# Performance work log

Hardware: AMD Instinct MI355X
Metric: run time of the kernel (lower is better)

Reference implementation:

```python
import jax, jax.numpy as jnp
import numpy as np

B, S, D = 2, 2048, 1024
H = 16
HD = D // H  # head_dim = 64


def setup_inputs() -> dict:
    key = jax.random.key(0)
    ks = jax.random.split(key, 9)
    sc_in = 1.0 / np.sqrt(D)
    return {
        "x": jax.random.normal(ks[0], (B, S, D), dtype=jnp.float32),
        "Wq": jax.random.normal(ks[1], (D, D), dtype=jnp.float32) * sc_in,
        "bq": jnp.zeros((D,), dtype=jnp.float32),
        "Wk": jax.random.normal(ks[2], (D, D), dtype=jnp.float32) * sc_in,
        "bk": jnp.zeros((D,), dtype=jnp.float32),
        "Wv": jax.random.normal(ks[3], (D, D), dtype=jnp.float32) * sc_in,
        "bv": jnp.zeros((D,), dtype=jnp.float32),
        "Wo": jax.random.normal(ks[4], (D, D), dtype=jnp.float32) * sc_in,
        "bo": jnp.zeros((D,), dtype=jnp.float32),
    }


def reference(x, Wq, bq, Wk, bk, Wv, bv, Wo, bo):
    # QKV projections: [B,S,D] -> [B,H,S,HD]
    def split_heads(t):
        return t.reshape(B, S, H, HD).transpose(0, 2, 1, 3)

    Q = split_heads(x @ Wq + bq)
    K = split_heads(x @ Wk + bk)
    V = split_heads(x @ Wv + bv)

    scale = 1.0 / np.sqrt(HD).astype(np.float32)
    scores = jnp.einsum("bhqd,bhkd->bhqk", Q, K) * scale  # [B,H,S,S]
    weights = jax.nn.softmax(scores, axis=-1)
    # dropout(p=0.1) is identity in eval mode
    attended = jnp.einsum("bhqk,bhkd->bhqd", weights, V)  # [B,H,S,HD]
    attended = attended.transpose(0, 2, 1, 3).reshape(B, S, D)
    return attended @ Wo + bo
```

## Files before the change

kernel.cpp:

```cpp
#include <hip/hip_runtime.h>
#include <hip/hip_bf16.h>


#define S_ 2048
#define D_ 1024
#define HD_ 64
#define LDSW 72
#define QSZ 4194304
#define LOG2E 1.44269504f

typedef __attribute__((ext_vector_type(8))) short bf16x8;
typedef __attribute__((ext_vector_type(4))) float f32x4;

static __device__ __forceinline__ short f2bs(float f) {
    __hip_bfloat16 h = __float2bfloat16(f);
    return *reinterpret_cast<short*>(&h);
}
static __device__ __forceinline__ float bs2f(short s) {
    __hip_bfloat16 h = *reinterpret_cast<__hip_bfloat16*>(&s);
    return __bfloat162float(h);
}
static __device__ __forceinline__ bf16x8 cvt8(const float* p) {
    f32x4 u0 = *(const f32x4*)p;
    f32x4 u1 = *(const f32x4*)(p + 4);
    bf16x8 r;
    r[0] = f2bs(u0[0]); r[1] = f2bs(u0[1]); r[2] = f2bs(u0[2]); r[3] = f2bs(u0[3]);
    r[4] = f2bs(u1[0]); r[5] = f2bs(u1[1]); r[6] = f2bs(u1[2]); r[7] = f2bs(u1[3]);
    return r;
}
static __device__ __forceinline__ void gld16(const void* g, void* l) {
    __builtin_amdgcn_global_load_lds(
        (const __attribute__((address_space(1))) unsigned int*)g,
        (__attribute__((address_space(3))) unsigned int*)l, 16, 0, 0);
}
static __device__ __forceinline__ int detect_f32(const unsigned int* __restrict__ xw) {
    const unsigned int w = xw[threadIdx.x & 63];
    const int e = (int)((w >> 7) & 0xFFu);
    unsigned long long m = __ballot(e >= 117 && e <= 130);
    return (__popcll(m) >= 32) ? 0 : 1;
}

__global__ __launch_bounds__(256) void prep(
    const void* __restrict__ x,
    const void* __restrict__ w0, const void* __restrict__ w1,
    const void* __restrict__ w2, const void* __restrict__ w3,
    short* __restrict__ Wt)
{
    __shared__ __align__(16) short Ts[64 * LDSW];
    const int f32in = detect_f32((const unsigned int*)x);
    const int idx = blockIdx.x;
    const int z = idx >> 8, bb = idx & 255;
    const void* W = z == 0 ? w0 : z == 1 ? w1 : z == 2 ? w2 : w3;
    short* O = Wt + (size_t)z * D_ * D_;
    const int k0 = (bb & 15) * 64, n0 = (bb >> 4) * 64;
    const int t = threadIdx.x;
    const int row = t >> 2, seg = t & 3;

    if (f32in) {
        const float* wg = (const float*)W + (size_t)(k0 + row) * D_ + n0;
        *(bf16x8*)&Ts[row * LDSW + seg * 8]      = cvt8(wg + seg * 8);
        *(bf16x8*)&Ts[row * LDSW + seg * 8 + 32] = cvt8(wg + seg * 8 + 32);
    } else {
        const short* wg = (const short*)W + (size_t)(k0 + row) * D_ + n0;
        *(bf16x8*)&Ts[row * LDSW + seg * 8]      = *(const bf16x8*)(wg + seg * 8);
        *(bf16x8*)&Ts[row * LDSW + seg * 8 + 32] = *(const bf16x8*)(wg + seg * 8 + 32);
    }
    __syncthreads();

    short* og = O + (size_t)(n0 + row) * D_ + k0;
    #pragma unroll
    for (int g = 0; g < 2; ++g) {
        const int ks = seg * 8 + g * 32;
        alignas(16) short tmp[8];
        #pragma unroll
        for (int i = 0; i < 8; ++i) tmp[i] = Ts[(ks + i) * LDSW + row];
        *(bf16x8*)(og + ks) = *(const bf16x8*)tmp;
    }
}

__global__ __launch_bounds__(256) void gemm_qkv(
    const void* __restrict__ X, const short* __restrict__ Wt3,
    const void* __restrict__ bq, const void* __restrict__ bk,
    const void* __restrict__ bv, short* __restrict__ out)
{
    __shared__ __align__(16) short As[128 * 64];
    __shared__ __align__(16) short Bs[128 * 64];
    const int ext_f32 = detect_f32((const unsigned int*)X);
    const int t = threadIdx.x;
    const int wave = t >> 6, lane = t & 63;
    const int quad = lane >> 4, l16 = lane & 15;
    const int wm = wave & 1, wn = wave >> 1;
    const int m0 = blockIdx.x * 128, n0 = blockIdx.y * 128;
    const int id = n0 >> 10;
    const int lr = lane >> 3;
    const int kx = ((lane & 7) ^ (lr & 7)) * 8;

    f32x4 acc[4][4];
    #pragma unroll
    for (int i = 0; i < 4; ++i)
        #pragma unroll
        for (int j = 0; j < 4; ++j) acc[i][j] = (f32x4){0.f, 0.f, 0.f, 0.f};

    const size_t arow = (size_t)(m0 + wave * 32 + lr) * D_ + kx;
    const short* Bb = Wt3 + (size_t)(n0 + wave * 32 + lr) * D_ + kx;

    for (int kb = 0; kb < 16; ++kb) {
        __syncthreads();
        const int k0 = kb * 64;
        if (ext_f32) {
            const float* Xf = (const float*)X;
            #pragma unroll
            for (int i = 0; i < 4; ++i)
                *(bf16x8*)&As[(wave * 4 + i) * 512 + lane * 8] =
                    cvt8(Xf + arow + (size_t)i * 8 * D_ + k0);
        } else {
            const short* Xs = (const short*)X;
            #pragma unroll
            for (int i = 0; i < 4; ++i)
                gld16(Xs + arow + (size_t)i * 8 * D_ + k0, &As[(wave * 4 + i) * 512]);
        }
        #pragma unroll
        for (int i = 0; i < 4; ++i)
            gld16(Bb + (size_t)i * 8 * D_ + k0, &Bs[(wave * 4 + i) * 512]);
        __syncthreads();

        #pragma unroll
        for (int ks = 0; ks < 2; ++ks) {
            const int sw = ((ks * 4 + quad) ^ (l16 & 7)) * 8;
            bf16x8 af[4], bfr[4];
            #pragma unroll
            for (int i = 0; i < 4; ++i) {
                af[i]  = *(const bf16x8*)&As[(wm * 64 + i * 16 + l16) * 64 + sw];
                bfr[i] = *(const bf16x8*)&Bs[(wn * 64 + i * 16 + l16) * 64 + sw];
            }
            #pragma unroll
            for (int mi = 0; mi < 4; ++mi)
                #pragma unroll
                for (int ni = 0; ni < 4; ++ni)
                    acc[mi][ni] = __builtin_amdgcn_mfma_f32_16x16x32_bf16(
                        af[mi], bfr[ni], acc[mi][ni], 0, 0, 0);
        }
    }

    const void* bias = id == 0 ? bq : id == 1 ? bk : bv;
    const float oscale = id == 0 ? 0.125f : 1.0f;
    #pragma unroll
    for (int ni = 0; ni < 4; ++ni) {
        const int n = n0 + wn * 64 + ni * 16 + l16;
        const int nl = n & 1023, h = nl >> 6, d = nl & 63;
        const float bvl = ext_f32 ? ((const float*)bias)[nl]
                                  : bs2f(((const short*)bias)[nl]);
        #pragma unroll
        for (int mi = 0; mi < 4; ++mi)
            #pragma unroll
            for (int r = 0; r < 4; ++r) {
                const int m = m0 + wm * 64 + mi * 16 + quad * 4 + r;
                const int b = m >> 11, s = m & 2047;
                const int bh = b * 16 + h;
                const float v = (acc[mi][ni][r] + bvl) * oscale;
                const size_t idx = (id < 2)
                    ? (size_t)id * QSZ + ((size_t)bh * S_ + s) * HD_ + d
                    : (size_t)2 * QSZ + ((size_t)bh * HD_ + d) * S_ + s;
                out[idx] = f2bs(v);
            }
    }
}

__global__ __launch_bounds__(256) void gemm_out(
    const short* __restrict__ A, const short* __restrict__ Bt,
    const void* __restrict__ bias, void* __restrict__ C,
    const unsigned int* __restrict__ xw)
{
    __shared__ __align__(16) short As[64 * 64];
    __shared__ __align__(16) short Bs[128 * 64];
    const int ext_f32 = detect_f32(xw);
    const int t = threadIdx.x;
    const int wave = t >> 6, lane = t & 63;
    const int quad = lane >> 4, l16 = lane & 15;
    const int wm = wave & 1, wn = wave >> 1;
    const int m0 = blockIdx.x * 64, n0 = blockIdx.y * 128;
    const int lr = lane >> 3;
    const int kx = ((lane & 7) ^ (lr & 7)) * 8;

    f32x4 acc[2][4];
    #pragma unroll
    for (int i = 0; i < 2; ++i)
        #pragma unroll
        for (int j = 0; j < 4; ++j) acc[i][j] = (f32x4){0.f, 0.f, 0.f, 0.f};

    const short* Ab = A  + (size_t)(m0 + wave * 16 + lr) * D_ + kx;
    const short* Bb = Bt + (size_t)(n0 + wave * 32 + lr) * D_ + kx;

    for (int kb = 0; kb < 16; ++kb) {
        __syncthreads();
        const int k0 = kb * 64;
        #pragma unroll
        for (int i = 0; i < 2; ++i)
            gld16(Ab + (size_t)i * 8 * D_ + k0, &As[(wave * 2 + i) * 512]);
        #pragma unroll
        for (int i = 0; i < 4; ++i)
            gld16(Bb + (size_t)i * 8 * D_ + k0, &Bs[(wave * 4 + i) * 512]);
        __syncthreads();

        #pragma unroll
        for (int ks = 0; ks < 2; ++ks) {
            const int sw = ((ks * 4 + quad) ^ (l16 & 7)) * 8;
            bf16x8 af[2], bfr[4];
            #pragma unroll
            for (int i = 0; i < 2; ++i)
                af[i] = *(const bf16x8*)&As[(wm * 32 + i * 16 + l16) * 64 + sw];
            #pragma unroll
            for (int i = 0; i < 4; ++i)
                bfr[i] = *(const bf16x8*)&Bs[(wn * 64 + i * 16 + l16) * 64 + sw];
            #pragma unroll
            for (int mi = 0; mi < 2; ++mi)
                #pragma unroll
                for (int ni = 0; ni < 4; ++ni)
                    acc[mi][ni] = __builtin_amdgcn_mfma_f32_16x16x32_bf16(
                        af[mi], bfr[ni], acc[mi][ni], 0, 0, 0);
        }
    }

    #pragma unroll
    for (int ni = 0; ni < 4; ++ni) {
        const int n = n0 + wn * 64 + ni * 16 + l16;
        const float bvl = ext_f32 ? ((const float*)bias)[n]
                                  : bs2f(((const short*)bias)[n]);
        #pragma unroll
        for (int mi = 0; mi < 2; ++mi)
            #pragma unroll
            for (int r = 0; r < 4; ++r) {
                const int m = m0 + wm * 32 + mi * 16 + quad * 4 + r;
                const float v = acc[mi][ni][r] + bvl;
                const size_t idx = (size_t)m * D_ + n;
                if (ext_f32) ((float*)C)[idx] = v;
                else         ((short*)C)[idx] = f2bs(v);
            }
    }
}

__global__ __launch_bounds__(256) void attn(
    const short* __restrict__ Q, const short* __restrict__ K,
    const short* __restrict__ Vt, short* __restrict__ Aout)
{
    __shared__ __align__(16) short Ks[64 * 64];
    __shared__ __align__(16) short Vs[64 * 64];
    __shared__ __align__(16) short Ps[4][32 * LDSW];

    const int t = threadIdx.x;
    const int wave = t >> 6, lane = t & 63;
    const int quad = lane >> 4, l16 = lane & 15;
    const int bh = blockIdx.x;
    const int q0 = blockIdx.y * 128;
    const int lr = lane >> 3;
    const int kx = ((lane & 7) ^ (lr & 7)) * 8;
    short* pw = &Ps[wave][0];

    bf16x8 bq[2][2];
    #pragma unroll
    for (int mi = 0; mi < 2; ++mi) {
        const short* qr = Q + ((size_t)bh * S_ + q0 + wave * 32 + mi * 16 + l16) * HD_ + quad * 8;
        bq[mi][0] = *(const bf16x8*)qr;
        bq[mi][1] = *(const bf16x8*)(qr + 32);
    }

    bf16x8 ones;
    #pragma unroll
    for (int i = 0; i < 8; ++i) ones[i] = (short)0x3F80;

    f32x4 o[2][4], lacc[2];
    #pragma unroll
    for (int mi = 0; mi < 2; ++mi) {
        lacc[mi] = (f32x4){0.f, 0.f, 0.f, 0.f};
        #pragma unroll
        for (int nt = 0; nt < 4; ++nt) o[mi][nt] = (f32x4){0.f, 0.f, 0.f, 0.f};
    }

    const short* Kb = K  + ((size_t)bh * S_  + wave * 16 + lr) * HD_ + kx;
    const short* Vb = Vt + ((size_t)bh * HD_ + wave * 16 + lr) * S_ + kx;

    for (int j = 0; j < 32; ++j) {
        __syncthreads();
        #pragma unroll
        for (int i = 0; i < 2; ++i) {
            gld16(Kb + ((size_t)j * 64 + i * 8) * HD_, &Ks[(wave * 2 + i) * 512]);
            gld16(Vb + (size_t)i * 8 * S_ + j * 64,    &Vs[(wave * 2 + i) * 512]);
        }
        __syncthreads();

        f32x4 st[2][4];
        #pragma unroll
        for (int nt = 0; nt < 4; ++nt) {
            bf16x8 kf0 = *(const bf16x8*)&Ks[(nt * 16 + l16) * 64 + ((quad ^ (l16 & 7)) * 8)];
            bf16x8 kf1 = *(const bf16x8*)&Ks[(nt * 16 + l16) * 64 + (((4 + quad) ^ (l16 & 7)) * 8)];
            #pragma unroll
            for (int mi = 0; mi < 2; ++mi) {
                f32x4 z = (f32x4){0.f, 0.f, 0.f, 0.f};
                z = __builtin_amdgcn_mfma_f32_16x16x32_bf16(kf0, bq[mi][0], z, 0, 0, 0);
                z = __builtin_amdgcn_mfma_f32_16x16x32_bf16(kf1, bq[mi][1], z, 0, 0, 0);
                st[mi][nt] = z;
            }
        }

        #pragma unroll
        for (int mi = 0; mi < 2; ++mi)
            #pragma unroll
            for (int nt = 0; nt < 4; ++nt) {
                unsigned u0 = __float_as_uint(__builtin_amdgcn_exp2f(st[mi][nt][0] * LOG2E));
                unsigned u1 = __float_as_uint(__builtin_amdgcn_exp2f(st[mi][nt][1] * LOG2E));
                unsigned u2 = __float_as_uint(__builtin_amdgcn_exp2f(st[mi][nt][2] * LOG2E));
                unsigned u3 = __float_as_uint(__builtin_amdgcn_exp2f(st[mi][nt][3] * LOG2E));
                uint2 pk;
                pk.x = __builtin_amdgcn_perm(u1, u0, 0x07060302);
                pk.y = __builtin_amdgcn_perm(u3, u2, 0x07060302);
                *(uint2*)&pw[(mi * 16 + l16) * LDSW + nt * 16 + quad * 4] = pk;
            }
        __builtin_amdgcn_s_waitcnt(0xc07f);

        #pragma unroll
        for (int ks = 0; ks < 2; ++ks) {
            bf16x8 vf[4];
            #pragma unroll
            for (int nt = 0; nt < 4; ++nt)
                vf[nt] = *(const bf16x8*)&Vs[(nt * 16 + l16) * 64 + (((ks * 4 + quad) ^ (l16 & 7)) * 8)];
            #pragma unroll
            for (int mi = 0; mi < 2; ++mi) {
                bf16x8 ap = *(const bf16x8*)&pw[(mi * 16 + l16) * LDSW + ks * 32 + quad * 8];
                lacc[mi] = __builtin_amdgcn_mfma_f32_16x16x32_bf16(ap, ones, lacc[mi], 0, 0, 0);
                #pragma unroll
                for (int nt = 0; nt < 4; ++nt)
                    o[mi][nt] = __builtin_amdgcn_mfma_f32_16x16x32_bf16(ap, vf[nt], o[mi][nt], 0, 0, 0);
            }
        }
    }

    const int b = bh >> 4, h = bh & 15;
    #pragma unroll
    for (int mi = 0; mi < 2; ++mi)
        #pragma unroll
        for (int r = 0; r < 4; ++r) {
            const float inv = 1.f / lacc[mi][r];
            const int s = q0 + wave * 32 + mi * 16 + quad * 4 + r;
            const size_t base = ((size_t)b * S_ + s) * D_ + h * HD_;
            #pragma unroll
            for (int nt = 0; nt < 4; ++nt)
                Aout[base + nt * 16 + l16] = f2bs(o[mi][nt][r] * inv);
        }
}

extern "C" void kernel_launch(void* const* d_in, const int* in_sizes, int n_in,
                              void* d_out, int out_size, void* d_ws, size_t ws_size,
                              hipStream_t stream) {
    char* ws = (char*)d_ws;
    short* Wt  = (short*)(ws + ((size_t)1  << 20));
    short* Att = (short*)(ws + ((size_t)9  << 20));
    short* QKV = (short*)(ws + ((size_t)17 << 20));
    const unsigned int* xw = (const unsigned int*)d_in[0];

    prep<<<1024, 256, 0, stream>>>(d_in[0], d_in[1], d_in[3], d_in[5], d_in[7], Wt);
    gemm_qkv<<<dim3(32, 24), 256, 0, stream>>>(d_in[0], Wt, d_in[2], d_in[4], d_in[6], QKV);
    attn<<<dim3(32, 16), 256, 0, stream>>>(QKV, QKV + QSZ, QKV + 2 * QSZ, Att);
    gemm_out<<<dim3(64, 8), 256, 0, stream>>>(Att, Wt + (3 << 20), d_in[8], d_out, xw);
}
```

Baseline: 190.5 us.

## Double-buffer K/V tiles in attention, use 8 waves, fold log2e into Q scale

The attention kernel now runs 512 threads per block, with each wave owning 16 query rows instead of 32. K and V tiles are double-buffered in shared memory so the next tile's global load is issued before compute on the current one, which leaves one barrier per iteration. The log2(e) factor is folded into the Q projection scale, removing a multiply per exponent. The cost is twice the LDS for K/V, fewer MFMAs per wave relative to its K/V fragment loads, and more waves competing for registers and LDS.

New measurement: 188.8 us (median of 2 runs). About the same (-0.9%).

```diff
diff --git a/kernel.cpp b/kernel.cpp
--- a/kernel.cpp
+++ b/kernel.cpp
@@ -7,7 +7,6 @@
 #define HD_ 64
 #define LDSW 72
 #define QSZ 4194304
-#define LOG2E 1.44269504f
 
 typedef __attribute__((ext_vector_type(8))) short bf16x8;
 typedef __attribute__((ext_vector_type(4))) float f32x4;
@@ -143,7 +142,7 @@
     }
 
     const void* bias = id == 0 ? bq : id == 1 ? bk : bv;
-    const float oscale = id == 0 ? 0.125f : 1.0f;
+    const float oscale = id == 0 ? 0.18033688011112042f : 1.0f;
     #pragma unroll
     for (int ni = 0; ni < 4; ++ni) {
         const int n = n0 + wn * 64 + ni * 16 + l16;
@@ -239,13 +238,13 @@
     }
 }
 
-__global__ __launch_bounds__(256) void attn(
+__global__ __launch_bounds__(512) void attn(
     const short* __restrict__ Q, const short* __restrict__ K,
     const short* __restrict__ Vt, short* __restrict__ Aout)
 {
-    __shared__ __align__(16) short Ks[64 * 64];
-    __shared__ __align__(16) short Vs[64 * 64];
-    __shared__ __align__(16) short Ps[4][32 * LDSW];
+    __shared__ __align__(16) short Ks[2][64 * 64];
+    __shared__ __align__(16) short Vs[2][64 * 64];
+    __shared__ __align__(16) short Ps[8][16 * LDSW];
 
     const int t = threadIdx.x;
     const int wave = t >> 6, lane = t & 63;
@@ -256,65 +255,58 @@
     const int kx = ((lane & 7) ^ (lr & 7)) * 8;
     short* pw = &Ps[wave][0];
 
-    bf16x8 bq[2][2];
-    #pragma unroll
-    for (int mi = 0; mi < 2; ++mi) {
-        const short* qr = Q + ((size_t)bh * S_ + q0 + wave * 32 + mi * 16 + l16) * HD_ + quad * 8;
-        bq[mi][0] = *(const bf16x8*)qr;
-        bq[mi][1] = *(const bf16x8*)(qr + 32);
+    bf16x8 bq0, bq1;
+    {
+        const short* qr = Q + ((size_t)bh * S_ + q0 + wave * 16 + l16) * HD_ + quad * 8;
+        bq0 = *(const bf16x8*)qr;
+        bq1 = *(const bf16x8*)(qr + 32);
     }
 
     bf16x8 ones;
     #pragma unroll
     for (int i = 0; i < 8; ++i) ones[i] = (short)0x3F80;
 
-    f32x4 o[2][4], lacc[2];
-    #pragma unroll
-    for (int mi = 0; mi < 2; ++mi) {
-        lacc[mi] = (f32x4){0.f, 0.f, 0.f, 0.f};
-        #pragma unroll
-        for (int nt = 0; nt < 4; ++nt) o[mi][nt] = (f32x4){0.f, 0.f, 0.f, 0.f};
-    }
-
-    const short* Kb = K  + ((size_t)bh * S_  + wave * 16 + lr) * HD_ + kx;
-    const short* Vb = Vt + ((size_t)bh * HD_ + wave * 16 + lr) * S_ + kx;
+    f32x4 o[4], lacc;
+    lacc = (f32x4){0.f, 0.f, 0.f, 0.f};
+    #pragma unroll
+    for (int nt = 0; nt < 4; ++nt) o[nt] = (f32x4){0.f, 0.f, 0.f, 0.f};
+
+    const short* Kb = K  + ((size_t)bh * S_  + wave * 8 + lr) * HD_ + kx;
+    const short* Vb = Vt + ((size_t)bh * HD_ + wave * 8 + lr) * S_ + kx;
+
+    gld16(Kb, &Ks[0][wave * 512]);
+    gld16(Vb, &Vs[0][wave * 512]);
+    __syncthreads();
 
     for (int j = 0; j < 32; ++j) {
-        __syncthreads();
-        #pragma unroll
-        for (int i = 0; i < 2; ++i) {
-            gld16(Kb + ((size_t)j * 64 + i * 8) * HD_, &Ks[(wave * 2 + i) * 512]);
-            gld16(Vb + (size_t)i * 8 * S_ + j * 64,    &Vs[(wave * 2 + i) * 512]);
-        }
-        __syncthreads();
-
-        f32x4 st[2][4];
+        const int cur = j & 1;
+        if (j < 31) {
+            gld16(Kb + (size_t)((j + 1) * 64) * HD_, &Ks[cur ^ 1][wave * 512]);
+            gld16(Vb + (j + 1) * 64,                 &Vs[cur ^ 1][wave * 512]);
+        }
+
+        f32x4 st[4];
         #pragma unroll
         for (int nt = 0; nt < 4; ++nt) {
-            bf16x8 kf0 = *(const bf16x8*)&Ks[(nt * 16 + l16) * 64 + ((quad ^ (l16 & 7)) * 8)];
-            bf16x8 kf1 = *(const bf16x8*)&Ks[(nt * 16 + l16) * 64 + (((4 + quad) ^ (l16 & 7)) * 8)];
-            #pragma unroll
-            for (int mi = 0; mi < 2; ++mi) {
-                f32x4 z = (f32x4){0.f, 0.f, 0.f, 0.f};
-                z = __builtin_amdgcn_mfma_f32_16x16x32_bf16(kf0, bq[mi][0], z, 0, 0, 0);
-                z = __builtin_amdgcn_mfma_f32_16x16x32_bf16(kf1, bq[mi][1], z, 0, 0, 0);
-                st[mi][nt] = z;
-            }
-        }
-
-        #pragma unroll
-        for (int mi = 0; mi < 2; ++mi)
-            #pragma unroll
-            for (int nt = 0; nt < 4; ++nt) {
-                unsigned u0 = __float_as_uint(__builtin_amdgcn_exp2f(st[mi][nt][0] * LOG2E));
-                unsigned u1 = __float_as_uint(__builtin_amdgcn_exp2f(st[mi][nt][1] * LOG2E));
-                unsigned u2 = __float_as_uint(__builtin_amdgcn_exp2f(st[mi][nt][2] * LOG2E));
-                unsigned u3 = __float_as_uint(__builtin_amdgcn_exp2f(st[mi][nt][3] * LOG2E));
-                uint2 pk;
-                pk.x = __builtin_amdgcn_perm(u1, u0, 0x07060302);
-                pk.y = __builtin_amdgcn_perm(u3, u2, 0x07060302);
-                *(uint2*)&pw[(mi * 16 + l16) * LDSW + nt * 16 + quad * 4] = pk;
-            }
+            bf16x8 kf0 = *(const bf16x8*)&Ks[cur][(nt * 16 + l16) * 64 + ((quad ^ (l16 & 7)) * 8)];
+            bf16x8 kf1 = *(const bf16x8*)&Ks[cur][(nt * 16 + l16) * 64 + (((4 + quad) ^ (l16 & 7)) * 8)];
+            f32x4 z = (f32x4){0.f, 0.f, 0.f, 0.f};
+            z = __builtin_amdgcn_mfma_f32_16x16x32_bf16(kf0, bq0, z, 0, 0, 0);
+            z = __builtin_amdgcn_mfma_f32_16x16x32_bf16(kf1, bq1, z, 0, 0, 0);
+            st[nt] = z;
+        }
+
+        #pragma unroll
+        for (int nt = 0; nt < 4; ++nt) {
+            unsigned u0 = __float_as_uint(__builtin_amdgcn_exp2f(st[nt][0]));
+            unsigned u1 = __float_as_uint(__builtin_amdgcn_exp2f(st[nt][1]));
+            unsigned u2 = __float_as_uint(__builtin_amdgcn_exp2f(st[nt][2]));
+            unsigned u3 = __float_as_uint(__builtin_amdgcn_exp2f(st[nt][3]));
+            uint2 pk;
+            pk.x = __builtin_amdgcn_perm(u1, u0, 0x07060302);
+            pk.y = __builtin_amdgcn_perm(u3, u2, 0x07060302);
+            *(uint2*)&pw[l16 * LDSW + nt * 16 + quad * 4] = pk;
+        }
         __builtin_amdgcn_s_waitcnt(0xc07f);
 
         #pragma unroll
@@ -322,30 +314,27 @@
             bf16x8 vf[4];
             #pragma unroll
             for (int nt = 0; nt < 4; ++nt)
-                vf[nt] = *(const bf16x8*)&Vs[(nt * 16 + l16) * 64 + (((ks * 4 + quad) ^ (l16 & 7)) * 8)];
-            #pragma unroll
-            for (int mi = 0; mi < 2; ++mi) {
-                bf16x8 ap = *(const bf16x8*)&pw[(mi * 16 + l16) * LDSW + ks * 32 + quad * 8];
-                lacc[mi] = __builtin_amdgcn_mfma_f32_16x16x32_bf16(ap, ones, lacc[mi], 0, 0, 0);
-                #pragma unroll
-                for (int nt = 0; nt < 4; ++nt)
-                    o[mi][nt] = __builtin_amdgcn_mfma_f32_16x16x32_bf16(ap, vf[nt], o[mi][nt], 0, 0, 0);
-            }
-        }
+                vf[nt] = *(const bf16x8*)&Vs[cur][(nt * 16 + l16) * 64 + (((ks * 4 + quad) ^ (l16 & 7)) * 8)];
+            bf16x8 ap = *(const bf16x8*)&pw[l16 * LDSW + ks * 32 + quad * 8];
+            lacc = __builtin_amdgcn_mfma_f32_16x16x32_bf16(ap, ones, lacc, 0, 0, 0);
+            #pragma unroll
+            for (int nt = 0; nt < 4; ++nt)
+                o[nt] = __builtin_amdgcn_mfma_f32_16x16x32_bf16(ap, vf[nt], o[nt], 0, 0, 0);
+        }
+
+        __syncthreads();
     }
 
     const int b = bh >> 4, h = bh & 15;
     #pragma unroll
-    for (int mi = 0; mi < 2; ++mi)
-        #pragma unroll
-        for (int r = 0; r < 4; ++r) {
-            const float inv = 1.f / lacc[mi][r];
-            const int s = q0 + wave * 32 + mi * 16 + quad * 4 + r;
-            const size_t base = ((size_t)b * S_ + s) * D_ + h * HD_;
-            #pragma unroll
-            for (int nt = 0; nt < 4; ++nt)
-                Aout[base + nt * 16 + l16] = f2bs(o[mi][nt][r] * inv);
-        }
+    for (int r = 0; r < 4; ++r) {
+        const float inv = 1.f / lacc[r];
+        const int s = q0 + wave * 16 + quad * 4 + r;
+        const size_t base = ((size_t)b * S_ + s) * D_ + h * HD_;
+        #pragma unroll
+        for (int nt = 0; nt < 4; ++nt)
+            Aout[base + nt * 16 + l16] = f2bs(o[nt][r] * inv);
+    }
 }
 
 extern "C" void kernel_launch(void* const* d_in, const int* in_sizes, int n_in,
@@ -359,6 +348,6 @@
 
     prep<<<1024, 256, 0, stream>>>(d_in[0], d_in[1], d_in[3], d_in[5], d_in[7], Wt);
     gemm_qkv<<<dim3(32, 24), 256, 0, stream>>>(d_in[0], Wt, d_in[2], d_in[4], d_in[6], QKV);
-    attn<<<dim3(32, 16), 256, 0, stream>>>(QKV, QKV + QSZ, QKV + 2 * QSZ, Att);
+    attn<<<dim3(32, 16), 512, 0, stream>>>(QKV, QKV + QSZ, QKV + 2 * QSZ, Att);
     gemm_out<<<dim3(64, 8), 256, 0, stream>>>(Att, Wt + (3 << 20), d_in[8], d_out, xw);
 }
```

## Double-buffer K/V tiles and feed P from registers via 16x16x16 MFMA

Applied to the files above, without the earlier changes.

The attention loop now double-buffers the K and V tiles in LDS, prefetching the next tile while the current one is computed, and uses one barrier per iteration instead of two. The softmax numerator P is no longer staged through LDS. The S^T=K·Q layout is used directly as the A operand of 16x16x16 bf16 MFMAs, which removes the per-wave P buffer, its store/load and the waitcnt. The log2(e) factor is folded into the Q projection scale so the exp2 no longer needs a multiply. In exchange there are twice as many (smaller) MFMA instructions for PV and the row sums, and twice the LDS for K/V.

Result: slower. 201.1 us (+5.6%).

```diff
diff --git a/kernel.cpp b/kernel.cpp
--- a/kernel.cpp
+++ b/kernel.cpp
@@ -7,9 +7,9 @@
 #define HD_ 64
 #define LDSW 72
 #define QSZ 4194304
-#define LOG2E 1.44269504f
 
 typedef __attribute__((ext_vector_type(8))) short bf16x8;
+typedef __attribute__((ext_vector_type(4))) short bf16x4;
 typedef __attribute__((ext_vector_type(4))) float f32x4;
 
 static __device__ __forceinline__ short f2bs(float f) {
@@ -27,6 +27,14 @@
     r[0] = f2bs(u0[0]); r[1] = f2bs(u0[1]); r[2] = f2bs(u0[2]); r[3] = f2bs(u0[3]);
     r[4] = f2bs(u1[0]); r[5] = f2bs(u1[1]); r[6] = f2bs(u1[2]); r[7] = f2bs(u1[3]);
     return r;
+}
+static __device__ __forceinline__ f32x4 pmfma(bf16x4 a, bf16x4 b, f32x4 c) {
+#if __has_builtin(__builtin_amdgcn_mfma_f32_16x16x16bf16_1k)
+    return __builtin_amdgcn_mfma_f32_16x16x16bf16_1k(a, b, c, 0, 0, 0);
+#else
+    asm("v_mfma_f32_16x16x16_bf16 %0, %1, %2, %0" : "+v"(c) : "v"(a), "v"(b));
+    return c;
+#endif
 }
 static __device__ __forceinline__ void gld16(const void* g, void* l) {
     __builtin_amdgcn_global_load_lds(
@@ -143,7 +151,7 @@
     }
 
     const void* bias = id == 0 ? bq : id == 1 ? bk : bv;
-    const float oscale = id == 0 ? 0.125f : 1.0f;
+    const float oscale = id == 0 ? 0.18033688011112042f : 1.0f;
     #pragma unroll
     for (int ni = 0; ni < 4; ++ni) {
         const int n = n0 + wn * 64 + ni * 16 + l16;
@@ -243,9 +251,8 @@
     const short* __restrict__ Q, const short* __restrict__ K,
     const short* __restrict__ Vt, short* __restrict__ Aout)
 {
-    __shared__ __align__(16) short Ks[64 * 64];
-    __shared__ __align__(16) short Vs[64 * 64];
-    __shared__ __align__(16) short Ps[4][32 * LDSW];
+    __shared__ __align__(16) short Ks[2][64 * 64];
+    __shared__ __align__(16) short Vs[2][64 * 64];
 
     const int t = threadIdx.x;
     const int wave = t >> 6, lane = t & 63;
@@ -254,7 +261,8 @@
     const int q0 = blockIdx.y * 128;
     const int lr = lane >> 3;
     const int kx = ((lane & 7) ^ (lr & 7)) * 8;
-    short* pw = &Ps[wave][0];
+    const int x7 = l16 & 7;
+    const int qh = quad >> 1, ql = (quad & 1) * 4;
 
     bf16x8 bq[2][2];
     #pragma unroll
@@ -264,9 +272,9 @@
         bq[mi][1] = *(const bf16x8*)(qr + 32);
     }
 
-    bf16x8 ones;
-    #pragma unroll
-    for (int i = 0; i < 8; ++i) ones[i] = (short)0x3F80;
+    bf16x4 ones4;
+    #pragma unroll
+    for (int i = 0; i < 4; ++i) ones4[i] = (short)0x3F80;
 
     f32x4 o[2][4], lacc[2];
     #pragma unroll
@@ -279,59 +287,64 @@
     const short* Kb = K  + ((size_t)bh * S_  + wave * 16 + lr) * HD_ + kx;
     const short* Vb = Vt + ((size_t)bh * HD_ + wave * 16 + lr) * S_ + kx;
 
+    #pragma unroll
+    for (int i = 0; i < 2; ++i) {
+        gld16(Kb + (size_t)i * 8 * HD_, &Ks[0][(wave * 2 + i) * 512]);
+        gld16(Vb + (size_t)i * 8 * S_,  &Vs[0][(wave * 2 + i) * 512]);
+    }
+    __syncthreads();
+
     for (int j = 0; j < 32; ++j) {
-        __syncthreads();
-        #pragma unroll
-        for (int i = 0; i < 2; ++i) {
-            gld16(Kb + ((size_t)j * 64 + i * 8) * HD_, &Ks[(wave * 2 + i) * 512]);
-            gld16(Vb + (size_t)i * 8 * S_ + j * 64,    &Vs[(wave * 2 + i) * 512]);
-        }
-        __syncthreads();
-
-        f32x4 st[2][4];
+        const int cur = j & 1;
+        if (j < 31) {
+            #pragma unroll
+            for (int i = 0; i < 2; ++i) {
+                gld16(Kb + (size_t)((j + 1) * 64 + i * 8) * HD_, &Ks[cur ^ 1][(wave * 2 + i) * 512]);
+                gld16(Vb + (size_t)i * 8 * S_ + (j + 1) * 64,    &Vs[cur ^ 1][(wave * 2 + i) * 512]);
+            }
+        }
+        const short* Kc = &Ks[cur][0];
+        const short* Vc = &Vs[cur][0];
+
+        bf16x4 pa[2][4];
         #pragma unroll
         for (int nt = 0; nt < 4; ++nt) {
-            bf16x8 kf0 = *(const bf16x8*)&Ks[(nt * 16 + l16) * 64 + ((quad ^ (l16 & 7)) * 8)];
-            bf16x8 kf1 = *(const bf16x8*)&Ks[(nt * 16 + l16) * 64 + (((4 + quad) ^ (l16 & 7)) * 8)];
+            bf16x8 kf0 = *(const bf16x8*)&Kc[(nt * 16 + l16) * 64 + ((quad ^ x7) * 8)];
+            bf16x8 kf1 = *(const bf16x8*)&Kc[(nt * 16 + l16) * 64 + (((4 + quad) ^ x7) * 8)];
             #pragma unroll
             for (int mi = 0; mi < 2; ++mi) {
                 f32x4 z = (f32x4){0.f, 0.f, 0.f, 0.f};
                 z = __builtin_amdgcn_mfma_f32_16x16x32_bf16(kf0, bq[mi][0], z, 0, 0, 0);
                 z = __builtin_amdgcn_mfma_f32_16x16x32_bf16(kf1, bq[mi][1], z, 0, 0, 0);
-                st[mi][nt] = z;
-            }
-        }
-
-        #pragma unroll
-        for (int mi = 0; mi < 2; ++mi)
-            #pragma unroll
-            for (int nt = 0; nt < 4; ++nt) {
-                unsigned u0 = __float_as_uint(__builtin_amdgcn_exp2f(st[mi][nt][0] * LOG2E));
-                unsigned u1 = __float_as_uint(__builtin_amdgcn_exp2f(st[mi][nt][1] * LOG2E));
-                unsigned u2 = __float_as_uint(__builtin_amdgcn_exp2f(st[mi][nt][2] * LOG2E));
-                unsigned u3 = __float_as_uint(__builtin_amdgcn_exp2f(st[mi][nt][3] * LOG2E));
+                unsigned u0 = __float_as_uint(__builtin_amdgcn_exp2f(z[0]));
+                unsigned u1 = __float_as_uint(__builtin_amdgcn_exp2f(z[1]));
+                unsigned u2 = __float_as_uint(__builtin_amdgcn_exp2f(z[2]));
+                unsigned u3 = __float_as_uint(__builtin_amdgcn_exp2f(z[3]));
                 uint2 pk;
                 pk.x = __builtin_amdgcn_perm(u1, u0, 0x07060302);
                 pk.y = __builtin_amdgcn_perm(u3, u2, 0x07060302);
-                *(uint2*)&pw[(mi * 16 + l16) * LDSW + nt * 16 + quad * 4] = pk;
-            }
-        __builtin_amdgcn_s_waitcnt(0xc07f);
-
-        #pragma unroll
-        for (int ks = 0; ks < 2; ++ks) {
-            bf16x8 vf[4];
+                pa[mi][nt] = *(bf16x4*)&pk;
+            }
+        }
+
+        #pragma unroll
+        for (int mi = 0; mi < 2; ++mi)
             #pragma unroll
             for (int nt = 0; nt < 4; ++nt)
-                vf[nt] = *(const bf16x8*)&Vs[(nt * 16 + l16) * 64 + (((ks * 4 + quad) ^ (l16 & 7)) * 8)];
-            #pragma unroll
-            for (int mi = 0; mi < 2; ++mi) {
-                bf16x8 ap = *(const bf16x8*)&pw[(mi * 16 + l16) * LDSW + ks * 32 + quad * 8];
-                lacc[mi] = __builtin_amdgcn_mfma_f32_16x16x32_bf16(ap, ones, lacc[mi], 0, 0, 0);
-                #pragma unroll
-                for (int nt = 0; nt < 4; ++nt)
-                    o[mi][nt] = __builtin_amdgcn_mfma_f32_16x16x32_bf16(ap, vf[nt], o[mi][nt], 0, 0, 0);
-            }
-        }
+                lacc[mi] = pmfma(pa[mi][nt], ones4, lacc[mi]);
+
+        #pragma unroll
+        for (int ntd = 0; ntd < 4; ++ntd) {
+            const int ro = (ntd * 16 + l16) * 64;
+            #pragma unroll
+            for (int ntk = 0; ntk < 4; ++ntk) {
+                bf16x4 vb = *(const bf16x4*)&Vc[ro + (((ntk * 2 + qh) ^ x7) * 8) + ql];
+                o[0][ntd] = pmfma(pa[0][ntk], vb, o[0][ntd]);
+                o[1][ntd] = pmfma(pa[1][ntk], vb, o[1][ntd]);
+            }
+        }
+
+        __syncthreads();
     }
 
     const int b = bh >> 4, h = bh & 15;
```
